# Kernel tuning notes

Hardware: AMD Instinct MI355X
Metric: run time of the kernel (lower is better)

## Reference

```python
import jax, jax.numpy as jnp
import numpy as np

D_MODEL = 1024
BULK_DIM = 10          # int(log2(d_model))
ADS_RADIUS = 1.0
B, N = 4, 2048


def setup_inputs() -> dict:
    key = jax.random.key(0)
    k1, k2 = jax.random.split(key, 2)
    boundary_tokens = jax.random.normal(k1, (B, N, D_MODEL), dtype=jnp.float32)
    W_b2b = jax.random.normal(k2, (D_MODEL, D_MODEL * BULK_DIM), dtype=jnp.float32) / np.sqrt(D_MODEL).astype(np.float32)
    b_b2b = jnp.zeros((D_MODEL * BULK_DIM,), dtype=jnp.float32)
    return {"boundary_tokens": boundary_tokens, "W_b2b": W_b2b, "b_b2b": b_b2b}


def _fast_marching(bulk_coords, ads_radius):
    # bulk_coords: (B, N, K, D). Sequential eikonal-style sweep through the
    # bulk depth z = 1..K; AdS warp factor L/z attenuates the front update
    # deeper into the bulk. Returns geodesics with the same shape.
    cz = jnp.moveaxis(bulk_coords, 2, 0)                 # (K, B, N, D)
    z = jnp.arange(1, bulk_coords.shape[2] + 1, dtype=bulk_coords.dtype)
    factors = ads_radius / z                             # (K,)

    def step(g, inp):
        c, f = inp
        g_new = g + f * (c - g)
        return g_new, g_new

    _, geos = jax.lax.scan(step, cz[0], (cz, factors))   # (K, B, N, D)
    return jnp.moveaxis(geos, 0, 2)                      # (B, N, K, D)


def reference(boundary_tokens, W_b2b, b_b2b):
    Bb, Nn, D = boundary_tokens.shape
    # boundary -> bulk linear projection, reshaped to (B, N, bulk_dim, D)
    bulk_coords = (boundary_tokens @ W_b2b + b_b2b).reshape(Bb, Nn, BULK_DIM, D)
    geodesics = _fast_marching(bulk_coords, ADS_RADIUS)  # (B, N, K, D)
    bulk_features = geodesics.mean(axis=2)               # (B, N, D)
    return bulk_features
```

## Files before the change

### kernel.cpp

```cpp
#include <hip/hip_runtime.h>
#include <stdint.h>


static constexpr float FW[10] = {
    0.2928968253968254f, 0.1928968253968254f, 0.1428968253968254f,
    0.1095634920634921f, 0.0845634920634921f, 0.0645634920634921f,
    0.0478968253968254f, 0.0336111111111111f, 0.0211111111111111f,
    0.0100000000000000f};

typedef __attribute__((ext_vector_type(8))) short short8;
typedef __attribute__((ext_vector_type(4))) float floatx4;
typedef __attribute__((ext_vector_type(16))) float floatx16;

__device__ inline unsigned int bf16pack2(float hi, float lo) {
    unsigned int uh = __float_as_uint(hi) + 0x8000u;
    unsigned int ul = __float_as_uint(lo) + 0x8000u;
    return __builtin_amdgcn_perm(uh, ul, 0x07060302u);
}

#define LDS_AS(p) ((__attribute__((address_space(3))) unsigned int*)(p))
#define GLB_AS(p) ((const __attribute__((address_space(1))) unsigned int*)(p))

__global__ __launch_bounds__(256) void prep(const float* __restrict__ W,
                                            const float* __restrict__ tokens,
                                            const float* __restrict__ b,
                                            unsigned short* __restrict__ Wt,
                                            float* __restrict__ beff,
                                            uint4* __restrict__ Ab,
                                            int do_cvt) {
    __shared__ float T[32 * 65];
    const int t = threadIdx.x;
    const int bid = blockIdx.x;

    if (bid < 512) {
        const int n0 = (bid & 15) * 64;
        const int k0 = (bid >> 4) * 32;
#pragma unroll
        for (int s = 0; s < 2; ++s) {
            int slot = s * 256 + t;
            int r = slot >> 4;
            int c4 = (slot & 15) * 4;
            const float4* src = (const float4*)(W + (size_t)(k0 + r) * 10240 + n0 + c4);
            float4 acc = {0.f, 0.f, 0.f, 0.f};
#pragma unroll
            for (int j = 0; j < 10; ++j) {
                float4 v = src[j * 256];
                acc.x += FW[j] * v.x; acc.y += FW[j] * v.y;
                acc.z += FW[j] * v.z; acc.w += FW[j] * v.w;
            }
            T[r * 65 + c4 + 0] = acc.x;
            T[r * 65 + c4 + 1] = acc.y;
            T[r * 65 + c4 + 2] = acc.z;
            T[r * 65 + c4 + 3] = acc.w;
        }
        __syncthreads();
#pragma unroll
        for (int s = 0; s < 2; ++s) {
            int slot = s * 256 + t;
            int nl = slot >> 3;
            int k4 = (slot & 7) * 4;
            float f0 = T[(k4 + 0) * 65 + nl];
            float f1 = T[(k4 + 1) * 65 + nl];
            float f2 = T[(k4 + 2) * 65 + nl];
            float f3 = T[(k4 + 3) * 65 + nl];
            uint2 p;
            p.x = bf16pack2(f1, f0);
            p.y = bf16pack2(f3, f2);
            *(uint2*)(Wt + (size_t)(n0 + nl) * 1024 + k0 + k4) = p;
        }
        return;
    }
    if (bid == 512) {
        const float4* src = (const float4*)b + t;
        float4 acc = {0.f, 0.f, 0.f, 0.f};
#pragma unroll
        for (int j = 0; j < 10; ++j) {
            float4 v = src[j * 256];
            acc.x += FW[j] * v.x; acc.y += FW[j] * v.y;
            acc.z += FW[j] * v.z; acc.w += FW[j] * v.w;
        }
        ((float4*)beff)[t] = acc;
        return;
    }
    if (do_cvt) {
        size_t i = (size_t)(bid - 513) * 256 + t;
        const float4* src = (const float4*)tokens + i * 2;
        float4 a0 = src[0], a1 = src[1];
        uint4 p;
        p.x = bf16pack2(a0.y, a0.x);
        p.y = bf16pack2(a0.w, a0.z);
        p.z = bf16pack2(a1.y, a1.x);
        p.w = bf16pack2(a1.w, a1.z);
        Ab[i] = p;
    }
}

__global__ __launch_bounds__(256) void gemm32(const unsigned short* __restrict__ Ab,
                                              const unsigned short* __restrict__ Wt,
                                              const float* __restrict__ beff,
                                              float* __restrict__ C) {
    __shared__ __align__(16) unsigned char As[2][16384];
    __shared__ __align__(16) unsigned char Bs[2][16384];

    const int t = threadIdx.x;
    const int lane = t & 63;
    const int w = t >> 6;
    const int l31 = lane & 31;
    const int khalf = lane >> 5;
    const int wm = (w & 1) * 64;
    const int wn = (w >> 1) * 64;
    const int bm = blockIdx.x * 128;
    const int bn = blockIdx.y * 128;

    floatx16 acc[2][2];
#pragma unroll
    for (int i = 0; i < 2; ++i)
#pragma unroll
        for (int j = 0; j < 2; ++j)
#pragma unroll
            for (int r = 0; r < 16; ++r) acc[i][j][r] = 0.f;

    const char* Abase = (const char*)Ab + (size_t)bm * 2048;
    const char* Bbase = (const char*)Wt + (size_t)bn * 2048;

    const int sI = w * 4;

#pragma unroll
    for (int i = 0; i < 4; ++i) {
        int I = sI + i;
        int slot = I * 64 + lane;
        int m = slot >> 3;
        int c = (slot & 7) ^ (m & 7);
        size_t off = (size_t)m * 2048 + c * 16;
        __builtin_amdgcn_global_load_lds(GLB_AS(Abase + off), LDS_AS(As[0] + I * 1024), 16, 0, 0);
        __builtin_amdgcn_global_load_lds(GLB_AS(Bbase + off), LDS_AS(Bs[0] + I * 1024), 16, 0, 0);
    }

#pragma unroll
    for (int kt = 0; kt < 16; ++kt) {
        __syncthreads();

        if (kt < 15) {
            int k0n = (kt + 1) * 64;
            int buf = (kt + 1) & 1;
#pragma unroll
            for (int i = 0; i < 4; ++i) {
                int I = sI + i;
                int slot = I * 64 + lane;
                int m = slot >> 3;
                int c = (slot & 7) ^ (m & 7);
                size_t off = (size_t)m * 2048 + (size_t)k0n * 2 + c * 16;
                __builtin_amdgcn_global_load_lds(GLB_AS(Abase + off), LDS_AS(As[buf] + I * 1024), 16, 0, 0);
                __builtin_amdgcn_global_load_lds(GLB_AS(Bbase + off), LDS_AS(Bs[buf] + I * 1024), 16, 0, 0);
            }
        }

        const unsigned char* Acur = As[kt & 1];
        const unsigned char* Bcur = Bs[kt & 1];
#pragma unroll
        for (int kk = 0; kk < 4; ++kk) {
            int c = kk * 2 + khalf;
            short8 af[2], bf[2];
#pragma unroll
            for (int tm = 0; tm < 2; ++tm) {
                int m = wm + tm * 32 + l31;
                int slot = m * 8 + (c ^ (m & 7));
                af[tm] = *(const short8*)(Acur + slot * 16);
            }
#pragma unroll
            for (int tn = 0; tn < 2; ++tn) {
                int n = wn + tn * 32 + l31;
                int slot = n * 8 + (c ^ (n & 7));
                bf[tn] = *(const short8*)(Bcur + slot * 16);
            }
#pragma unroll
            for (int tm = 0; tm < 2; ++tm)
#pragma unroll
                for (int tn = 0; tn < 2; ++tn)
                    acc[tm][tn] = __builtin_amdgcn_mfma_f32_32x32x16_bf16(
                        af[tm], bf[tn], acc[tm][tn], 0, 0, 0);
        }
    }

#pragma unroll
    for (int tn = 0; tn < 2; ++tn) {
        int col = bn + wn + tn * 32 + l31;
        float bias = beff[col];
#pragma unroll
        for (int tm = 0; tm < 2; ++tm) {
            int rbase = bm + wm + tm * 32 + 4 * khalf;
#pragma unroll
            for (int r = 0; r < 16; ++r) {
                int row = rbase + (r & 3) + 8 * (r >> 2);
                C[(size_t)row * 1024 + col] = acc[tm][tn][r] + bias;
            }
        }
    }
}

__global__ __launch_bounds__(256) void gemm_fb(const float* __restrict__ A,
                                               const unsigned short* __restrict__ Wt,
                                               const float* __restrict__ beff,
                                               float* __restrict__ C) {
    __shared__ __align__(16) unsigned short As[128 * 72];
    __shared__ __align__(16) unsigned char Bs[16384];

    const int t = threadIdx.x;
    const int lane = t & 63;
    const int w = t >> 6;
    const int quad = lane >> 4;
    const int l15 = lane & 15;
    const int wm = (w & 1) * 64;
    const int wn = (w >> 1) * 64;
    const int bm = blockIdx.y * 128;
    const int bn = blockIdx.x * 128;

    floatx4 acc[4][4];
#pragma unroll
    for (int i = 0; i < 4; ++i)
#pragma unroll
        for (int j = 0; j < 4; ++j) acc[i][j] = (floatx4){0.f, 0.f, 0.f, 0.f};

    const int ar = t >> 4;
    const int ac4 = (t & 15) * 4;
    const float* Abase = A + (size_t)(bm + ar) * 1024 + ac4;
    const char* WtB = (const char*)Wt;

    for (int k0 = 0; k0 < 1024; k0 += 64) {
#pragma unroll
        for (int i = 0; i < 4; ++i) {
            int I = w * 4 + i;
            int slot = I * 64 + lane;
            int nl = slot >> 3;
            int c = (slot & 7) ^ (nl & 7);
            const char* g = WtB + (size_t)(bn + nl) * 2048 + k0 * 2 + c * 16;
            __builtin_amdgcn_global_load_lds(GLB_AS(g), LDS_AS(Bs + I * 1024), 16, 0, 0);
        }
        float4 av[8];
#pragma unroll
        for (int s = 0; s < 8; ++s)
            av[s] = *(const float4*)(Abase + (size_t)(s * 16) * 1024 + k0);
#pragma unroll
        for (int s = 0; s < 8; ++s) {
            uint2 p;
            p.x = bf16pack2(av[s].y, av[s].x);
            p.y = bf16pack2(av[s].w, av[s].z);
            *(uint2*)((char*)As + (size_t)(s * 16 + ar) * 144 + ac4 * 2) = p;
        }
        __syncthreads();
#pragma unroll
        for (int kk = 0; kk < 2; ++kk) {
            short8 af[4], bf[4];
#pragma unroll
            for (int tm = 0; tm < 4; ++tm) {
                int m = wm + tm * 16 + l15;
                af[tm] = *(const short8*)((const char*)As + (size_t)m * 144 + kk * 64 + quad * 16);
            }
#pragma unroll
            for (int tn = 0; tn < 4; ++tn) {
                int n = wn + tn * 16 + l15;
                int c = kk * 4 + quad;
                int slot = n * 8 + (c ^ (n & 7));
                bf[tn] = *(const short8*)(Bs + slot * 16);
            }
#pragma unroll
            for (int tm = 0; tm < 4; ++tm)
#pragma unroll
                for (int tn = 0; tn < 4; ++tn)
                    acc[tm][tn] = __builtin_amdgcn_mfma_f32_16x16x32_bf16(
                        af[tm], bf[tn], acc[tm][tn], 0, 0, 0);
        }
        __syncthreads();
    }
#pragma unroll
    for (int tn = 0; tn < 4; ++tn) {
        int col = bn + wn + tn * 16 + l15;
        float bias = beff[col];
#pragma unroll
        for (int tm = 0; tm < 4; ++tm) {
            int row0 = bm + wm + tm * 16 + quad * 4;
#pragma unroll
            for (int r = 0; r < 4; ++r)
                C[(size_t)(row0 + r) * 1024 + col] = acc[tm][tn][r] + bias;
        }
    }
}

extern "C" void kernel_launch(void* const* d_in, const int* in_sizes, int n_in,
                              void* d_out, int out_size, void* d_ws, size_t ws_size,
                              hipStream_t stream) {
    const float* tokens = (const float*)d_in[0];
    const float* W      = (const float*)d_in[1];
    const float* b      = (const float*)d_in[2];
    float* out = (float*)d_out;

    unsigned short* Wt = (unsigned short*)d_ws;
    float* beff = (float*)((char*)d_ws + 2097152);
    unsigned short* Ab = (unsigned short*)((char*)d_ws + 2101248);

    const int big_ws = ws_size >= 2101248 + (size_t)8192 * 1024 * 2;

    if (big_ws) {
        prep<<<513 + 4096, 256, 0, stream>>>(W, tokens, b, Wt, beff, (uint4*)Ab, 1);
        gemm32<<<dim3(64, 8), 256, 0, stream>>>(Ab, Wt, beff, out);
    } else {
        prep<<<513, 256, 0, stream>>>(W, tokens, b, Wt, beff, (uint4*)Ab, 0);
        gemm_fb<<<dim3(8, 64), 256, 0, stream>>>(tokens, Wt, beff, out);
    }
}
```

Baseline: 129.7 us.

## Fuse fp32-to-bf16 activation conversion into the 32x32 MFMA GEMM load pipeline

Removes the separate pass in prep that converted the fp32 tokens to a bf16 workspace buffer. The GEMM now loads fp32 A tiles into registers, keeps the direct-to-LDS loads for the weights, and packs A to bf16 into the swizzled LDS buffer after the MFMA work of each step, so the global loads overlap compute. This avoids writing and re-reading a 16 MB intermediate, but doubles the global bytes read per A tile and adds register pressure and VALU packing inside the main loop. The small-workspace fallback GEMM is deleted.

```diff
diff --git a/kernel.cpp b/kernel.cpp
--- a/kernel.cpp
+++ b/kernel.cpp
@@ -9,7 +9,6 @@
     0.0100000000000000f};
 
 typedef __attribute__((ext_vector_type(8))) short short8;
-typedef __attribute__((ext_vector_type(4))) float floatx4;
 typedef __attribute__((ext_vector_type(16))) float floatx16;
 
 __device__ inline unsigned int bf16pack2(float hi, float lo) {
@@ -22,12 +21,9 @@
 #define GLB_AS(p) ((const __attribute__((address_space(1))) unsigned int*)(p))
 
 __global__ __launch_bounds__(256) void prep(const float* __restrict__ W,
-                                            const float* __restrict__ tokens,
                                             const float* __restrict__ b,
                                             unsigned short* __restrict__ Wt,
-                                            float* __restrict__ beff,
-                                            uint4* __restrict__ Ab,
-                                            int do_cvt) {
+                                            float* __restrict__ beff) {
     __shared__ float T[32 * 65];
     const int t = threadIdx.x;
     const int bid = blockIdx.x;
@@ -70,32 +66,18 @@
         }
         return;
     }
-    if (bid == 512) {
-        const float4* src = (const float4*)b + t;
-        float4 acc = {0.f, 0.f, 0.f, 0.f};
-#pragma unroll
-        for (int j = 0; j < 10; ++j) {
-            float4 v = src[j * 256];
-            acc.x += FW[j] * v.x; acc.y += FW[j] * v.y;
-            acc.z += FW[j] * v.z; acc.w += FW[j] * v.w;
-        }
-        ((float4*)beff)[t] = acc;
-        return;
-    }
-    if (do_cvt) {
-        size_t i = (size_t)(bid - 513) * 256 + t;
-        const float4* src = (const float4*)tokens + i * 2;
-        float4 a0 = src[0], a1 = src[1];
-        uint4 p;
-        p.x = bf16pack2(a0.y, a0.x);
-        p.y = bf16pack2(a0.w, a0.z);
-        p.z = bf16pack2(a1.y, a1.x);
-        p.w = bf16pack2(a1.w, a1.z);
-        Ab[i] = p;
-    }
-}
-
-__global__ __launch_bounds__(256) void gemm32(const unsigned short* __restrict__ Ab,
+    const float4* src = (const float4*)b + t;
+    float4 acc = {0.f, 0.f, 0.f, 0.f};
+#pragma unroll
+    for (int j = 0; j < 10; ++j) {
+        float4 v = src[j * 256];
+        acc.x += FW[j] * v.x; acc.y += FW[j] * v.y;
+        acc.z += FW[j] * v.z; acc.w += FW[j] * v.w;
+    }
+    ((float4*)beff)[t] = acc;
+}
+
+__global__ __launch_bounds__(256) void gemm32(const float* __restrict__ A,
                                               const unsigned short* __restrict__ Wt,
                                               const float* __restrict__ beff,
                                               float* __restrict__ C) {
@@ -120,38 +102,60 @@
 #pragma unroll
             for (int r = 0; r < 16; ++r) acc[i][j][r] = 0.f;
 
-    const char* Abase = (const char*)Ab + (size_t)bm * 2048;
+    const char* Abase = (const char*)A + (size_t)bm * 4096;
     const char* Bbase = (const char*)Wt + (size_t)bn * 2048;
 
     const int sI = w * 4;
-
-#pragma unroll
-    for (int i = 0; i < 4; ++i) {
-        int I = sI + i;
-        int slot = I * 64 + lane;
-        int m = slot >> 3;
-        int c = (slot & 7) ^ (m & 7);
-        size_t off = (size_t)m * 2048 + c * 16;
-        __builtin_amdgcn_global_load_lds(GLB_AS(Abase + off), LDS_AS(As[0] + I * 1024), 16, 0, 0);
-        __builtin_amdgcn_global_load_lds(GLB_AS(Bbase + off), LDS_AS(Bs[0] + I * 1024), 16, 0, 0);
+    int sm[4], sc[4];
+#pragma unroll
+    for (int i = 0; i < 4; ++i) {
+        int s = (sI + i) * 64 + lane;
+        sm[i] = s >> 3;
+        sc[i] = (s & 7) ^ (sm[i] & 7);
+    }
+
+    float4 ar[4][2];
+
+#pragma unroll
+    for (int i = 0; i < 4; ++i) {
+        const float4* ga = (const float4*)(Abase + (size_t)sm[i] * 4096 + sc[i] * 32);
+        ar[i][0] = ga[0];
+        ar[i][1] = ga[1];
+    }
+#pragma unroll
+    for (int i = 0; i < 4; ++i) {
+        __builtin_amdgcn_global_load_lds(GLB_AS(Bbase + (size_t)sm[i] * 2048 + sc[i] * 16),
+                                         LDS_AS(Bs[0] + (sI + i) * 1024), 16, 0, 0);
+    }
+#pragma unroll
+    for (int i = 0; i < 4; ++i) {
+        uint4 p;
+        p.x = bf16pack2(ar[i][0].y, ar[i][0].x);
+        p.y = bf16pack2(ar[i][0].w, ar[i][0].z);
+        p.z = bf16pack2(ar[i][1].y, ar[i][1].x);
+        p.w = bf16pack2(ar[i][1].w, ar[i][1].z);
+        *(uint4*)(As[0] + (sI + i) * 1024 + lane * 16) = p;
     }
 
 #pragma unroll
     for (int kt = 0; kt < 16; ++kt) {
         __syncthreads();
 
+        const int buf = (kt + 1) & 1;
         if (kt < 15) {
-            int k0n = (kt + 1) * 64;
-            int buf = (kt + 1) & 1;
+            const int k0n = (kt + 1) * 64;
 #pragma unroll
             for (int i = 0; i < 4; ++i) {
-                int I = sI + i;
-                int slot = I * 64 + lane;
-                int m = slot >> 3;
-                int c = (slot & 7) ^ (m & 7);
-                size_t off = (size_t)m * 2048 + (size_t)k0n * 2 + c * 16;
-                __builtin_amdgcn_global_load_lds(GLB_AS(Abase + off), LDS_AS(As[buf] + I * 1024), 16, 0, 0);
-                __builtin_amdgcn_global_load_lds(GLB_AS(Bbase + off), LDS_AS(Bs[buf] + I * 1024), 16, 0, 0);
+                const float4* ga = (const float4*)(Abase + (size_t)sm[i] * 4096 +
+                                                   (size_t)k0n * 4 + sc[i] * 32);
+                ar[i][0] = ga[0];
+                ar[i][1] = ga[1];
+            }
+#pragma unroll
+            for (int i = 0; i < 4; ++i) {
+                __builtin_amdgcn_global_load_lds(
+                    GLB_AS(Bbase + (size_t)sm[i] * 2048 + (size_t)k0n * 2 + sc[i] * 16),
+                    LDS_AS(Bs[buf] + (sI + i) * 1024), 16, 0, 0);
             }
         }
 
@@ -180,6 +184,18 @@
                     acc[tm][tn] = __builtin_amdgcn_mfma_f32_32x32x16_bf16(
                         af[tm], bf[tn], acc[tm][tn], 0, 0, 0);
         }
+
+        if (kt < 15) {
+#pragma unroll
+            for (int i = 0; i < 4; ++i) {
+                uint4 p;
+                p.x = bf16pack2(ar[i][0].y, ar[i][0].x);
+                p.y = bf16pack2(ar[i][0].w, ar[i][0].z);
+                p.z = bf16pack2(ar[i][1].y, ar[i][1].x);
+                p.w = bf16pack2(ar[i][1].w, ar[i][1].z);
+                *(uint4*)(As[buf] + (sI + i) * 1024 + lane * 16) = p;
+            }
+        }
     }
 
 #pragma unroll
@@ -194,94 +210,6 @@
                 int row = rbase + (r & 3) + 8 * (r >> 2);
                 C[(size_t)row * 1024 + col] = acc[tm][tn][r] + bias;
             }
-        }
-    }
-}
-
-__global__ __launch_bounds__(256) void gemm_fb(const float* __restrict__ A,
-                                               const unsigned short* __restrict__ Wt,
-                                               const float* __restrict__ beff,
-                                               float* __restrict__ C) {
-    __shared__ __align__(16) unsigned short As[128 * 72];
-    __shared__ __align__(16) unsigned char Bs[16384];
-
-    const int t = threadIdx.x;
-    const int lane = t & 63;
-    const int w = t >> 6;
-    const int quad = lane >> 4;
-    const int l15 = lane & 15;
-    const int wm = (w & 1) * 64;
-    const int wn = (w >> 1) * 64;
-    const int bm = blockIdx.y * 128;
-    const int bn = blockIdx.x * 128;
-
-    floatx4 acc[4][4];
-#pragma unroll
-    for (int i = 0; i < 4; ++i)
-#pragma unroll
-        for (int j = 0; j < 4; ++j) acc[i][j] = (floatx4){0.f, 0.f, 0.f, 0.f};
-
-    const int ar = t >> 4;
-    const int ac4 = (t & 15) * 4;
-    const float* Abase = A + (size_t)(bm + ar) * 1024 + ac4;
-    const char* WtB = (const char*)Wt;
-
-    for (int k0 = 0; k0 < 1024; k0 += 64) {
-#pragma unroll
-        for (int i = 0; i < 4; ++i) {
-            int I = w * 4 + i;
-            int slot = I * 64 + lane;
-            int nl = slot >> 3;
-            int c = (slot & 7) ^ (nl & 7);
-            const char* g = WtB + (size_t)(bn + nl) * 2048 + k0 * 2 + c * 16;
-            __builtin_amdgcn_global_load_lds(GLB_AS(g), LDS_AS(Bs + I * 1024), 16, 0, 0);
-        }
-        float4 av[8];
-#pragma unroll
-        for (int s = 0; s < 8; ++s)
-            av[s] = *(const float4*)(Abase + (size_t)(s * 16) * 1024 + k0);
-#pragma unroll
-        for (int s = 0; s < 8; ++s) {
-            uint2 p;
-            p.x = bf16pack2(av[s].y, av[s].x);
-            p.y = bf16pack2(av[s].w, av[s].z);
-            *(uint2*)((char*)As + (size_t)(s * 16 + ar) * 144 + ac4 * 2) = p;
-        }
-        __syncthreads();
-#pragma unroll
-        for (int kk = 0; kk < 2; ++kk) {
-            short8 af[4], bf[4];
-#pragma unroll
-            for (int tm = 0; tm < 4; ++tm) {
-                int m = wm + tm * 16 + l15;
-                af[tm] = *(const short8*)((const char*)As + (size_t)m * 144 + kk * 64 + quad * 16);
-            }
-#pragma unroll
-            for (int tn = 0; tn < 4; ++tn) {
-                int n = wn + tn * 16 + l15;
-                int c = kk * 4 + quad;
-                int slot = n * 8 + (c ^ (n & 7));
-                bf[tn] = *(const short8*)(Bs + slot * 16);
-            }
-#pragma unroll
-            for (int tm = 0; tm < 4; ++tm)
-#pragma unroll
-                for (int tn = 0; tn < 4; ++tn)
-                    acc[tm][tn] = __builtin_amdgcn_mfma_f32_16x16x32_bf16(
-                        af[tm], bf[tn], acc[tm][tn], 0, 0, 0);
-        }
-        __syncthreads();
-    }
-#pragma unroll
-    for (int tn = 0; tn < 4; ++tn) {
-        int col = bn + wn + tn * 16 + l15;
-        float bias = beff[col];
-#pragma unroll
-        for (int tm = 0; tm < 4; ++tm) {
-            int row0 = bm + wm + tm * 16 + quad * 4;
-#pragma unroll
-            for (int r = 0; r < 4; ++r)
-                C[(size_t)(row0 + r) * 1024 + col] = acc[tm][tn][r] + bias;
         }
     }
 }
@@ -296,15 +224,7 @@
 
     unsigned short* Wt = (unsigned short*)d_ws;
     float* beff = (float*)((char*)d_ws + 2097152);
-    unsigned short* Ab = (unsigned short*)((char*)d_ws + 2101248);
-
-    const int big_ws = ws_size >= 2101248 + (size_t)8192 * 1024 * 2;
-
-    if (big_ws) {
-        prep<<<513 + 4096, 256, 0, stream>>>(W, tokens, b, Wt, beff, (uint4*)Ab, 1);
-        gemm32<<<dim3(64, 8), 256, 0, stream>>>(Ab, Wt, beff, out);
-    } else {
-        prep<<<513, 256, 0, stream>>>(W, tokens, b, Wt, beff, (uint4*)Ab, 0);
-        gemm_fb<<<dim3(8, 64), 256, 0, stream>>>(tokens, Wt, beff, out);
-    }
-}
+
+    prep<<<513, 256, 0, stream>>>(W, b, Wt, beff);
+    gemm32<<<dim3(64, 8), 256, 0, stream>>>(tokens, Wt, beff, out);
+}
```

Result: slower. 138.3 us (+6.7%).

## Deepen gemm32 pipeline to four-stage 32-wide K tiles with explicit vmcnt waits

Applied to the files above, without the earlier changes.

The GEMM main loop moves from a double-buffered 64-wide K tile to a four-buffer ring of 32-wide K tiles, issuing three stages of async global-to-LDS loads ahead. Each step waits on a partial vmcnt count rather than a full __syncthreads drain. The LDS swizzle is reworked so that row pairs share a 128-byte line. The aim is to hide global memory latency behind MFMA work and cut barrier stalls. In exchange there are twice as many barriers per tile, and correctness now rests on hand-tuned waitcnt values and sched_barrier placement.

```diff
diff --git a/kernel.cpp b/kernel.cpp
--- a/kernel.cpp
+++ b/kernel.cpp
@@ -99,8 +99,8 @@
                                               const unsigned short* __restrict__ Wt,
                                               const float* __restrict__ beff,
                                               float* __restrict__ C) {
-    __shared__ __align__(16) unsigned char As[2][16384];
-    __shared__ __align__(16) unsigned char Bs[2][16384];
+    __shared__ __align__(16) unsigned char As[4][8192];
+    __shared__ __align__(16) unsigned char Bs[4][8192];
 
     const int t = threadIdx.x;
     const int lane = t & 63;
@@ -123,54 +123,66 @@
     const char* Abase = (const char*)Ab + (size_t)bm * 2048;
     const char* Bbase = (const char*)Wt + (size_t)bn * 2048;
 
-    const int sI = w * 4;
-
-#pragma unroll
-    for (int i = 0; i < 4; ++i) {
-        int I = sI + i;
-        int slot = I * 64 + lane;
-        int m = slot >> 3;
-        int c = (slot & 7) ^ (m & 7);
-        size_t off = (size_t)m * 2048 + c * 16;
-        __builtin_amdgcn_global_load_lds(GLB_AS(Abase + off), LDS_AS(As[0] + I * 1024), 16, 0, 0);
-        __builtin_amdgcn_global_load_lds(GLB_AS(Bbase + off), LDS_AS(Bs[0] + I * 1024), 16, 0, 0);
-    }
-
-#pragma unroll
-    for (int kt = 0; kt < 16; ++kt) {
-        __syncthreads();
-
-        if (kt < 15) {
-            int k0n = (kt + 1) * 64;
-            int buf = (kt + 1) & 1;
-#pragma unroll
-            for (int i = 0; i < 4; ++i) {
-                int I = sI + i;
-                int slot = I * 64 + lane;
-                int m = slot >> 3;
-                int c = (slot & 7) ^ (m & 7);
-                size_t off = (size_t)m * 2048 + (size_t)k0n * 2 + c * 16;
-                __builtin_amdgcn_global_load_lds(GLB_AS(Abase + off), LDS_AS(As[buf] + I * 1024), 16, 0, 0);
-                __builtin_amdgcn_global_load_lds(GLB_AS(Bbase + off), LDS_AS(Bs[buf] + I * 1024), 16, 0, 0);
-            }
-        }
-
-        const unsigned char* Acur = As[kt & 1];
-        const unsigned char* Bcur = Bs[kt & 1];
-#pragma unroll
-        for (int kk = 0; kk < 4; ++kk) {
-            int c = kk * 2 + khalf;
+    int sm[2], sc[2];
+#pragma unroll
+    for (int i = 0; i < 2; ++i) {
+        int s = (w * 2 + i) * 64 + lane;
+        int pair = s >> 3;
+        int q = (s & 7) ^ (pair & 7);
+        sm[i] = pair * 2 + (q & 1);
+        sc[i] = q >> 1;
+    }
+
+#define STAGE(KT)                                                                     \
+    {                                                                                 \
+        const size_t koff = (size_t)(KT) * 64;                                        \
+        unsigned char* Ad = As[(KT) & 3];                                             \
+        unsigned char* Bd = Bs[(KT) & 3];                                             \
+        _Pragma("unroll") for (int i = 0; i < 2; ++i) {                               \
+            int I = w * 2 + i;                                                        \
+            __builtin_amdgcn_global_load_lds(                                         \
+                GLB_AS(Abase + (size_t)sm[i] * 2048 + koff + sc[i] * 16),             \
+                LDS_AS(Ad + I * 1024), 16, 0, 0);                                     \
+            __builtin_amdgcn_global_load_lds(                                         \
+                GLB_AS(Bbase + (size_t)sm[i] * 2048 + koff + sc[i] * 16),             \
+                LDS_AS(Bd + I * 1024), 16, 0, 0);                                     \
+        }                                                                             \
+    }
+
+    STAGE(0)
+    STAGE(1)
+    STAGE(2)
+
+#pragma unroll
+    for (int kt = 0; kt < 32; ++kt) {
+        if (kt < 30)
+            asm volatile("s_waitcnt vmcnt(8)" ::: "memory");
+        else if (kt == 30)
+            asm volatile("s_waitcnt vmcnt(4)" ::: "memory");
+        else
+            asm volatile("s_waitcnt vmcnt(0)" ::: "memory");
+        __builtin_amdgcn_s_barrier();
+        __builtin_amdgcn_sched_barrier(0);
+
+        if (kt < 29) STAGE(kt + 3)
+        __builtin_amdgcn_sched_barrier(0);
+
+        const unsigned char* Acur = As[kt & 3];
+        const unsigned char* Bcur = Bs[kt & 3];
+#pragma unroll
+        for (int kk = 0; kk < 2; ++kk) {
+            int f = kk * 2 + khalf;
             short8 af[2], bf[2];
 #pragma unroll
             for (int tm = 0; tm < 2; ++tm) {
                 int m = wm + tm * 32 + l31;
-                int slot = m * 8 + (c ^ (m & 7));
+                int slot = (m >> 1) * 8 + ((2 * f + (m & 1)) ^ ((m >> 1) & 7));
                 af[tm] = *(const short8*)(Acur + slot * 16);
             }
 #pragma unroll
             for (int tn = 0; tn < 2; ++tn) {
                 int n = wn + tn * 32 + l31;
-                int slot = n * 8 + (c ^ (n & 7));
+                int slot = (n >> 1) * 8 + ((2 * f + (n & 1)) ^ ((n >> 1) & 7));
                 bf[tn] = *(const short8*)(Bcur + slot * 16);
             }
 #pragma unroll
@@ -180,7 +192,9 @@
                     acc[tm][tn] = __builtin_amdgcn_mfma_f32_32x32x16_bf16(
                         af[tm], bf[tn], acc[tm][tn], 0, 0, 0);
         }
-    }
+        __builtin_amdgcn_sched_barrier(0);
+    }
+#undef STAGE
 
 #pragma unroll
     for (int tn = 0; tn < 2; ++tn) {
@@ -202,8 +216,8 @@
                                                const unsigned short* __restrict__ Wt,
                                                const float* __restrict__ beff,
                                                float* __restrict__ C) {
-    __shared__ __align__(16) unsigned short As[128 * 72];
-    __shared__ __align__(16) unsigned char Bs[16384];
+    __shared__ __align__(16) unsigned short Asl[128 * 72];
+    __shared__ __align__(16) unsigned char Bsl[16384];
 
     const int t = threadIdx.x;
     const int lane = t & 63;
@@ -234,7 +248,7 @@
             int nl = slot >> 3;
             int c = (slot & 7) ^ (nl & 7);
             const char* g = WtB + (size_t)(bn + nl) * 2048 + k0 * 2 + c * 16;
-            __builtin_amdgcn_global_load_lds(GLB_AS(g), LDS_AS(Bs + I * 1024), 16, 0, 0);
+            __builtin_amdgcn_global_load_lds(GLB_AS(g), LDS_AS(Bsl + I * 1024), 16, 0, 0);
         }
         float4 av[8];
 #pragma unroll
@@ -245,7 +259,7 @@
             uint2 p;
             p.x = bf16pack2(av[s].y, av[s].x);
             p.y = bf16pack2(av[s].w, av[s].z);
-            *(uint2*)((char*)As + (size_t)(s * 16 + ar) * 144 + ac4 * 2) = p;
+            *(uint2*)((char*)Asl + (size_t)(s * 16 + ar) * 144 + ac4 * 2) = p;
         }
         __syncthreads();
 #pragma unroll
@@ -254,14 +268,14 @@
 #pragma unroll
             for (int tm = 0; tm < 4; ++tm) {
                 int m = wm + tm * 16 + l15;
-                af[tm] = *(const short8*)((const char*)As + (size_t)m * 144 + kk * 64 + quad * 16);
+                af[tm] = *(const short8*)((const char*)Asl + (size_t)m * 144 + kk * 64 + quad * 16);
             }
 #pragma unroll
             for (int tn = 0; tn < 4; ++tn) {
                 int n = wn + tn * 16 + l15;
                 int c = kk * 4 + quad;
                 int slot = n * 8 + (c ^ (n & 7));
-                bf[tn] = *(const short8*)(Bs + slot * 16);
+                bf[tn] = *(const short8*)(Bsl + slot * 16);
             }
 #pragma unroll
             for (int tm = 0; tm < 4; ++tm)
```

Result: slower. 133.2 us (+2.7%).
